# Performance work log

Measured on AMD Instinct MI355X. Metric: run time of the kernel, lower is better.

## Reference

```python
import jax, jax.numpy as jnp
import numpy as np

N_NODES = 10000
N_EDGES = 640000
IN_C = 128
OUT_C = 128
BOND_F = 16


def setup_inputs() -> dict:
    key = jax.random.key(0)
    ks = jax.random.split(key, 8)
    x = jax.random.normal(ks[0], (N_NODES, IN_C), dtype=jnp.float32)
    edge_attr = jax.random.normal(ks[1], (N_EDGES, BOND_F), dtype=jnp.float32)
    edge_weight = jax.random.uniform(ks[2], (N_EDGES, 1), dtype=jnp.float32)
    W_bond = jax.random.normal(ks[3], (BOND_F, IN_C), dtype=jnp.float32) * 0.1
    b_bond = jax.random.normal(ks[4], (IN_C,), dtype=jnp.float32) * 0.1
    W_lin = jax.random.normal(ks[5], (IN_C, OUT_C), dtype=jnp.float32) * 0.05
    b_lin = jax.random.normal(ks[6], (OUT_C,), dtype=jnp.float32) * 0.05
    edge_index = jax.random.randint(ks[7], (2, N_EDGES), 0, N_NODES, dtype=jnp.int32)
    return {"x": x, "edge_attr": edge_attr, "edge_weight": edge_weight,
            "W_bond": W_bond, "b_bond": b_bond, "W_lin": W_lin, "b_lin": b_lin,
            "edge_index": edge_index}


def _inv_sqrt_deg(idx, n, dtype):
    # degree via segment_sum of ones; inf (deg==0) mapped to 0
    deg = jax.ops.segment_sum(jnp.ones_like(idx, dtype=dtype), idx, num_segments=n)
    return jnp.where(deg > 0, jax.lax.rsqrt(jnp.maximum(deg, 1.0)) * (deg > 0), 0.0).astype(dtype)


def reference(x, edge_attr, edge_weight, W_bond, b_bond, W_lin, b_lin, edge_index):
    n = x.shape[0]
    # bond encoder: Linear on edge features -> [E, C]
    edge_emb = edge_attr @ W_bond + b_bond
    # append self-loops with zero edge embedding and unit edge weight
    sl = jnp.arange(n, dtype=edge_index.dtype)
    ei = jnp.concatenate([edge_index, jnp.stack([sl, sl])], axis=1)  # [2, E+N]
    emb = jnp.concatenate([edge_emb, jnp.zeros((n, edge_emb.shape[1]), edge_emb.dtype)], axis=0)
    ew = jnp.concatenate([edge_weight, jnp.ones((n, 1), edge_weight.dtype)], axis=0)
    row, col = ei[0], ei[1]
    norm = _inv_sqrt_deg(row, n, x.dtype)[row] * _inv_sqrt_deg(col, n, x.dtype)[col]
    # gather + GELU(exact/erf) + degree norm + edge weight, then scatter-sum
    msg = jax.nn.gelu(x[row] + emb, approximate=False) * norm[:, None] * ew
    out = jax.ops.segment_sum(msg, col, num_segments=n)  # [N, C]
    return out @ W_lin + b_lin
```

## Files before the change

kernel.cpp:

```cpp
#include <hip/hip_runtime.h>
#include <hip/hip_bf16.h>
#include <math.h>

#define N_NODES 10000
#define N_EDGES 640000
#define C 128
#define BF 16
#define MAXD 160

typedef int   iv4 __attribute__((ext_vector_type(4)));
typedef float fv4 __attribute__((ext_vector_type(4)));

__device__ __forceinline__ float2 bf2_to_f2(unsigned u) {
    union { unsigned x; float f; } lo, hi;
    lo.x = (u & 0xffffu) << 16;
    hi.x = u & 0xffff0000u;
    float2 r; r.x = lo.f; r.y = hi.f; return r;
}

__device__ __forceinline__ float fast_gelu(float z) {
    float z2 = z * z;
    float p  = z * fmaf(0.044715f, z2, 1.0f);
    float e  = __builtin_amdgcn_exp2f(-2.3022082f * p);
    float r  = __builtin_amdgcn_rcpf(1.0f + e);
    return z * r;
}

__global__ __launch_bounds__(256) void k_pre(
    const float* __restrict__ x, __hip_bfloat16* __restrict__ xb,
    const int* __restrict__ ei, int* __restrict__ dr, int* __restrict__ dc,
    int* __restrict__ pos)
{
    int b = blockIdx.x;
    if (b < 1250) {
        int i = (b * 256 + threadIdx.x) * 4;
        float4 v = *(const float4*)(x + i);
        xb[i + 0] = __float2bfloat16(v.x);
        xb[i + 1] = __float2bfloat16(v.y);
        xb[i + 2] = __float2bfloat16(v.z);
        xb[i + 3] = __float2bfloat16(v.w);
        return;
    }
    int e = (b - 1250) * 256 + threadIdx.x;
    int r = ei[e];
    int c = ei[N_EDGES + e];
    atomicAdd(&dr[r], 1);
    pos[e] = atomicAdd(&dc[c], 1);
}

__global__ __launch_bounds__(256) void k_prep2(
    const int* __restrict__ ei, const float* __restrict__ ew,
    const int* __restrict__ dr, const int* __restrict__ pos,
    iv4* __restrict__ bs)
{
    int e = blockIdx.x * 256 + threadIdx.x;
    int r = ei[e];
    int c = ei[N_EDGES + e];
    int pp = pos[e];
    if (pp >= MAXD) return;
    float s = rsqrtf((float)(dr[r] + 1)) * ew[e];
    iv4 v;
    v.x = e;
    v.y = r;
    v.z = __float_as_int(s);
    v.w = 0;
    bs[(size_t)c * MAXD + pp] = v;
}

#define EDGE_COMPUTE(q0, q1, q2, q3, xu, s) do {                          \
    float m0 = bbv.x, m1 = bbv.y;                                         \
    m0 = fmaf(q0.x, wb[0].x, m0);   m1 = fmaf(q0.x, wb[0].y, m1);         \
    m0 = fmaf(q0.y, wb[1].x, m0);   m1 = fmaf(q0.y, wb[1].y, m1);         \
    m0 = fmaf(q0.z, wb[2].x, m0);   m1 = fmaf(q0.z, wb[2].y, m1);         \
    m0 = fmaf(q0.w, wb[3].x, m0);   m1 = fmaf(q0.w, wb[3].y, m1);         \
    m0 = fmaf(q1.x, wb[4].x, m0);   m1 = fmaf(q1.x, wb[4].y, m1);         \
    m0 = fmaf(q1.y, wb[5].x, m0);   m1 = fmaf(q1.y, wb[5].y, m1);         \
    m0 = fmaf(q1.z, wb[6].x, m0);   m1 = fmaf(q1.z, wb[6].y, m1);         \
    m0 = fmaf(q1.w, wb[7].x, m0);   m1 = fmaf(q1.w, wb[7].y, m1);         \
    m0 = fmaf(q2.x, wb[8].x, m0);   m1 = fmaf(q2.x, wb[8].y, m1);         \
    m0 = fmaf(q2.y, wb[9].x, m0);   m1 = fmaf(q2.y, wb[9].y, m1);         \
    m0 = fmaf(q2.z, wb[10].x, m0);  m1 = fmaf(q2.z, wb[10].y, m1);        \
    m0 = fmaf(q2.w, wb[11].x, m0);  m1 = fmaf(q2.w, wb[11].y, m1);        \
    m0 = fmaf(q3.x, wb[12].x, m0);  m1 = fmaf(q3.x, wb[12].y, m1);        \
    m0 = fmaf(q3.y, wb[13].x, m0);  m1 = fmaf(q3.y, wb[13].y, m1);        \
    m0 = fmaf(q3.z, wb[14].x, m0);  m1 = fmaf(q3.z, wb[14].y, m1);        \
    m0 = fmaf(q3.w, wb[15].x, m0);  m1 = fmaf(q3.w, wb[15].y, m1);        \
    float2 xf = bf2_to_f2(xu);                                            \
    a0 = fmaf(fast_gelu(xf.x + m0), (s), a0);                             \
    a1 = fmaf(fast_gelu(xf.y + m1), (s), a1);                             \
} while (0)

__global__ __launch_bounds__(512) void k_node(
    const __hip_bfloat16* __restrict__ xb,
    const float* __restrict__ ea,
    const float* __restrict__ Wb, const float* __restrict__ bb,
    const int* __restrict__ dr, const int* __restrict__ dc,
    const iv4* __restrict__ bs,
    const float* __restrict__ Wl, const float* __restrict__ bl,
    float* __restrict__ out)
{
    int n = blockIdx.x;
    int t = threadIdx.x;
    int w = t >> 6;
    int p = t & 63;

    float2 wb[BF];
#pragma unroll
    for (int k = 0; k < BF; k++)
        wb[k] = *(const float2*)(Wb + (size_t)k * C + 2 * p);
    float2 bbv = *(const float2*)(bb + 2 * p);

    int cnt = dc[n]; if (cnt > MAXD) cnt = MAXD;
    float icn = rsqrtf((float)(dc[n] + 1));
    float irn = rsqrtf((float)(dr[n] + 1));

    float a0 = 0.f, a1 = 0.f;
    const unsigned* xbu = (const unsigned*)xb;
    int o0 = n * MAXD;
    int o1 = o0 + cnt;

    int i = o0 + w;
    if (i < o1) {
        iv4 h0 = __builtin_nontemporal_load(bs + i);
        iv4 h1 = (i + 8 < o1) ? __builtin_nontemporal_load(bs + i + 8) : h0;
        int e0 = __builtin_amdgcn_readfirstlane(h0.x);
        int r0 = __builtin_amdgcn_readfirstlane(h0.y);
        float s0 = __uint_as_float((unsigned)__builtin_amdgcn_readfirstlane(h0.z));
        const fv4* ep = (const fv4*)ea + (size_t)e0 * 4;
        fv4 q0 = ep[0], q1 = ep[1], q2 = ep[2], q3 = ep[3];
        unsigned xu = xbu[(size_t)r0 * 64 + p];

        while (true) {
            bool more = (i + 8 < o1);
            iv4 h2 = (i + 16 < o1) ? __builtin_nontemporal_load(bs + i + 16) : h0;
            int e1 = __builtin_amdgcn_readfirstlane(h1.x);
            int r1 = __builtin_amdgcn_readfirstlane(h1.y);
            float s1 = __uint_as_float((unsigned)__builtin_amdgcn_readfirstlane(h1.z));
            const fv4* epn = (const fv4*)ea + (size_t)e1 * 4;
            fv4 u0 = epn[0], u1 = epn[1], u2 = epn[2], u3 = epn[3];
            unsigned xun = xbu[(size_t)r1 * 64 + p];
            EDGE_COMPUTE(q0, q1, q2, q3, xu, s0);
            if (!more) break;
            q0 = u0; q1 = u1; q2 = u2; q3 = u3; xu = xun; s0 = s1;
            h0 = h1; h1 = h2; i += 8;
        }
    }

    __shared__ float2 shp[8][64];
    __shared__ __align__(16) float shs[C];
    __shared__ float sho[4][C];

    shp[w][p] = make_float2(a0, a1);
    __syncthreads();
    if (t < 64) {
        float vx = 0.f, vy = 0.f;
#pragma unroll
        for (int k = 0; k < 8; k++) { vx += shp[k][t].x; vy += shp[k][t].y; }
        float2 xf = bf2_to_f2(xbu[(size_t)n * 64 + t]);
        shs[2 * t]     = (vx + fast_gelu(xf.x) * irn) * icn;
        shs[2 * t + 1] = (vy + fast_gelu(xf.y) * irn) * icn;
    }
    __syncthreads();

    int ch = t & (C - 1), q = t >> 7;
    float o = 0.f;
    const float4* shv = (const float4*)shs + q * 8;
    const float* wcol = Wl + (size_t)(q * 32) * C + ch;
#pragma unroll
    for (int k4 = 0; k4 < 8; k4++) {
        float4 sv = shv[k4];
        o = fmaf(sv.x, wcol[(size_t)(k4 * 4 + 0) * C], o);
        o = fmaf(sv.y, wcol[(size_t)(k4 * 4 + 1) * C], o);
        o = fmaf(sv.z, wcol[(size_t)(k4 * 4 + 2) * C], o);
        o = fmaf(sv.w, wcol[(size_t)(k4 * 4 + 3) * C], o);
    }
    sho[q][ch] = o;
    __syncthreads();
    if (t < C) out[(size_t)n * C + t] = bl[t] + sho[0][t] + sho[1][t] + sho[2][t] + sho[3][t];
}

__global__ void k_deg(const int* __restrict__ ei, int* __restrict__ dr, int* __restrict__ dc) {
    int e = blockIdx.x * blockDim.x + threadIdx.x;
    if (e < N_EDGES) {
        atomicAdd(&dr[ei[e]], 1);
        atomicAdd(&dc[ei[N_EDGES + e]], 1);
    }
}

__global__ __launch_bounds__(1024) void k_scan_fb(
    const int* __restrict__ dr, const int* __restrict__ dc,
    int* __restrict__ off, float* __restrict__ ir, float* __restrict__ ic)
{
    __shared__ int shp[1024];
    int t = threadIdx.x;
    int base = t * 10;
    int loc[10];
    int s = 0;
#pragma unroll
    for (int j = 0; j < 10; j++) {
        int i = base + j;
        int v = (i < N_NODES) ? dc[i] : 0;
        loc[j] = s;
        s += v;
    }
    shp[t] = s;
    __syncthreads();
    for (int st = 1; st < 1024; st <<= 1) {
        int a = (t >= st) ? shp[t - st] : 0;
        __syncthreads();
        shp[t] += a;
        __syncthreads();
    }
    int excl = shp[t] - s;
#pragma unroll
    for (int j = 0; j < 10; j++) {
        int i = base + j;
        if (i < N_NODES) {
            off[i] = excl + loc[j];
            ir[i] = rsqrtf((float)(dr[i] + 1));
            ic[i] = rsqrtf((float)(dc[i] + 1));
        }
    }
    if (t == 1023) off[N_NODES] = shp[1023];
}

__global__ void k_scatter(const int* __restrict__ ei, const int* __restrict__ off,
                          int* __restrict__ cur, int* __restrict__ bucket) {
    int e = blockIdx.x * blockDim.x + threadIdx.x;
    if (e < N_EDGES) {
        int c = ei[N_EDGES + e];
        int pos = atomicAdd(&cur[c], 1);
        bucket[off[c] + pos] = e;
    }
}

__global__ __launch_bounds__(512) void k_node_fb(
    const float* __restrict__ x,
    const float* __restrict__ ea, const float* __restrict__ ew,
    const float* __restrict__ Wb, const float* __restrict__ bb,
    const int* __restrict__ ei,
    const float* __restrict__ ir, const float* __restrict__ ic,
    const int* __restrict__ off, const int* __restrict__ bucket,
    const float* __restrict__ Wl, const float* __restrict__ bl,
    float* __restrict__ out)
{
    int n = blockIdx.x;
    int t = threadIdx.x & (C - 1);
    int g = threadIdx.x >> 7;
    float icn = ic[n];
    float wb[BF];
#pragma unroll
    for (int k = 0; k < BF; k++) wb[k] = Wb[(size_t)k * C + t];
    float bbt = bb[t];
    float acc = 0.0f;
    if (g == 0) acc = fast_gelu(x[(size_t)n * C + t]) * (ir[n] * icn);
    int o0 = off[n], o1 = off[n + 1];
    for (int i = o0 + g; i < o1; i += 4) {
        int e = __builtin_amdgcn_readfirstlane(bucket[i]);
        int r = ei[e];
        float s = ir[r] * icn * ew[e];
        const float4* eapt = (const float4*)(ea + (size_t)e * BF);
        float4 q0 = eapt[0], q1 = eapt[1], q2 = eapt[2], q3 = eapt[3];
        float emb = bbt;
        emb = fmaf(q0.x, wb[0], emb);  emb = fmaf(q0.y, wb[1], emb);
        emb = fmaf(q0.z, wb[2], emb);  emb = fmaf(q0.w, wb[3], emb);
        emb = fmaf(q1.x, wb[4], emb);  emb = fmaf(q1.y, wb[5], emb);
        emb = fmaf(q1.z, wb[6], emb);  emb = fmaf(q1.w, wb[7], emb);
        emb = fmaf(q2.x, wb[8], emb);  emb = fmaf(q2.y, wb[9], emb);
        emb = fmaf(q2.z, wb[10], emb); emb = fmaf(q2.w, wb[11], emb);
        emb = fmaf(q3.x, wb[12], emb); emb = fmaf(q3.y, wb[13], emb);
        emb = fmaf(q3.z, wb[14], emb); emb = fmaf(q3.w, wb[15], emb);
        acc = fmaf(fast_gelu(x[(size_t)r * C + t] + emb), s, acc);
    }
    __shared__ float shp[4][C];
    __shared__ float shs[C];
    shp[g][t] = acc;
    __syncthreads();
    if (threadIdx.x < C) {
        int k = threadIdx.x;
        shs[k] = shp[0][k] + shp[1][k] + shp[2][k] + shp[3][k];
    }
    __syncthreads();
    float o = 0.0f;
    int k0 = g * 32;
#pragma unroll 8
    for (int j = 0; j < 32; j++) {
        int k = k0 + j;
        o = fmaf(shs[k], Wl[(size_t)k * C + t], o);
    }
    shp[g][t] = o;
    __syncthreads();
    if (threadIdx.x < C) {
        int c = threadIdx.x;
        out[(size_t)n * C + c] = bl[c] + shp[0][c] + shp[1][c] + shp[2][c] + shp[3][c];
    }
}

extern "C" void kernel_launch(void* const* d_in, const int* in_sizes, int n_in,
                              void* d_out, int out_size, void* d_ws, size_t ws_size,
                              hipStream_t stream) {
    const float* x  = (const float*)d_in[0];
    const float* ea = (const float*)d_in[1];
    const float* ew = (const float*)d_in[2];
    const float* Wb = (const float*)d_in[3];
    const float* bb = (const float*)d_in[4];
    const float* Wl = (const float*)d_in[5];
    const float* bl = (const float*)d_in[6];
    const int*   ei = (const int*)d_in[7];
    float* out = (float*)d_out;

    const size_t need_full = (size_t)N_NODES * MAXD * 16
                           + (size_t)640000 * 4 + (size_t)640000 * 4
                           + (size_t)2 * 10240 * 4;

    if (ws_size >= need_full) {
        iv4* bs = (iv4*)d_ws;
        unsigned* xbu = (unsigned*)(bs + (size_t)N_NODES * MAXD);
        int* pos = (int*)(xbu + 640000);
        int* dr  = pos + 640000;
        int* dc  = dr + 10240;
        __hip_bfloat16* xb = (__hip_bfloat16*)xbu;

        (void)hipMemsetAsync(dr, 0, 2 * 10240 * sizeof(int), stream);
        k_pre<<<3750, 256, 0, stream>>>(x, xb, ei, dr, dc, pos);
        k_prep2<<<2500, 256, 0, stream>>>(ei, ew, dr, pos, bs);
        k_node<<<N_NODES, 512, 0, stream>>>(
            xb, ea, Wb, bb, dr, dc, bs, Wl, bl, out);
    } else {
        int* bucket = (int*)d_ws;
        int* off = bucket + 640000;
        int* dr  = off + 10304;
        int* dc  = dr + 10240;
        int* cur = dc + 10240;
        float* ir = (float*)(cur + 10240);
        float* ic = ir + 10240;

        (void)hipMemsetAsync(dr, 0, 3 * 10240 * sizeof(int), stream);
        k_deg<<<(N_EDGES + 255) / 256, 256, 0, stream>>>(ei, dr, dc);
        k_scan_fb<<<1, 1024, 0, stream>>>(dr, dc, off, ir, ic);
        k_scatter<<<(N_EDGES + 255) / 256, 256, 0, stream>>>(ei, off, cur, bucket);
        k_node_fb<<<N_NODES, 512, 0, stream>>>(
            x, ea, ew, Wb, bb, ei, ir, ic, off, bucket, Wl, bl, out);
    }
}
```

Before: 271.3 us.

## Merge prep kernels, drop bf16 x copy, stage edge data in LDS

The degree-count and bucket-fill kernels become one, with the source-degree norm now applied inside the node kernel, so the separate pos array and one launch go away. The bf16 conversion of x is dropped and the node kernel gathers fp32 x directly. Each node block first loads its edge list and the matching edge_attr rows into shared memory cooperatively, then runs the per-edge loop out of LDS. The cost is double-width x gathers, extra syncthreads, and more LDS per block, which may lower occupancy.

```diff
diff --git a/kernel.cpp b/kernel.cpp
--- a/kernel.cpp
+++ b/kernel.cpp
@@ -8,15 +8,7 @@
 #define BF 16
 #define MAXD 160
 
-typedef int   iv4 __attribute__((ext_vector_type(4)));
-typedef float fv4 __attribute__((ext_vector_type(4)));
-
-__device__ __forceinline__ float2 bf2_to_f2(unsigned u) {
-    union { unsigned x; float f; } lo, hi;
-    lo.x = (u & 0xffffu) << 16;
-    hi.x = u & 0xffff0000u;
-    float2 r; r.x = lo.f; r.y = hi.f; return r;
-}
+typedef int iv4 __attribute__((ext_vector_type(4)));
 
 __device__ __forceinline__ float fast_gelu(float z) {
     float z2 = z * z;
@@ -26,48 +18,26 @@
     return z * r;
 }
 
-__global__ __launch_bounds__(256) void k_pre(
-    const float* __restrict__ x, __hip_bfloat16* __restrict__ xb,
-    const int* __restrict__ ei, int* __restrict__ dr, int* __restrict__ dc,
-    int* __restrict__ pos)
-{
-    int b = blockIdx.x;
-    if (b < 1250) {
-        int i = (b * 256 + threadIdx.x) * 4;
-        float4 v = *(const float4*)(x + i);
-        xb[i + 0] = __float2bfloat16(v.x);
-        xb[i + 1] = __float2bfloat16(v.y);
-        xb[i + 2] = __float2bfloat16(v.z);
-        xb[i + 3] = __float2bfloat16(v.w);
-        return;
-    }
-    int e = (b - 1250) * 256 + threadIdx.x;
-    int r = ei[e];
-    int c = ei[N_EDGES + e];
-    atomicAdd(&dr[r], 1);
-    pos[e] = atomicAdd(&dc[c], 1);
-}
-
-__global__ __launch_bounds__(256) void k_prep2(
+__global__ __launch_bounds__(256) void k_prep(
     const int* __restrict__ ei, const float* __restrict__ ew,
-    const int* __restrict__ dr, const int* __restrict__ pos,
-    iv4* __restrict__ bs)
+    int* __restrict__ dr, int* __restrict__ dc, iv4* __restrict__ bs)
 {
     int e = blockIdx.x * 256 + threadIdx.x;
     int r = ei[e];
     int c = ei[N_EDGES + e];
-    int pp = pos[e];
-    if (pp >= MAXD) return;
-    float s = rsqrtf((float)(dr[r] + 1)) * ew[e];
-    iv4 v;
-    v.x = e;
-    v.y = r;
-    v.z = __float_as_int(s);
-    v.w = 0;
-    bs[(size_t)c * MAXD + pp] = v;
-}
-
-#define EDGE_COMPUTE(q0, q1, q2, q3, xu, s) do {                          \
+    atomicAdd(&dr[r], 1);
+    int pp = atomicAdd(&dc[c], 1);
+    if (pp < MAXD) {
+        iv4 v;
+        v.x = e;
+        v.y = r;
+        v.z = __float_as_int(ew[e]);
+        v.w = 0;
+        bs[(size_t)c * MAXD + pp] = v;
+    }
+}
+
+#define EDGE_COMPUTE(q0, q1, q2, q3, xf, s) do {                          \
     float m0 = bbv.x, m1 = bbv.y;                                         \
     m0 = fmaf(q0.x, wb[0].x, m0);   m1 = fmaf(q0.x, wb[0].y, m1);         \
     m0 = fmaf(q0.y, wb[1].x, m0);   m1 = fmaf(q0.y, wb[1].y, m1);         \
@@ -85,14 +55,12 @@
     m0 = fmaf(q3.y, wb[13].x, m0);  m1 = fmaf(q3.y, wb[13].y, m1);        \
     m0 = fmaf(q3.z, wb[14].x, m0);  m1 = fmaf(q3.z, wb[14].y, m1);        \
     m0 = fmaf(q3.w, wb[15].x, m0);  m1 = fmaf(q3.w, wb[15].y, m1);        \
-    float2 xf = bf2_to_f2(xu);                                            \
     a0 = fmaf(fast_gelu(xf.x + m0), (s), a0);                             \
     a1 = fmaf(fast_gelu(xf.y + m1), (s), a1);                             \
 } while (0)
 
 __global__ __launch_bounds__(512) void k_node(
-    const __hip_bfloat16* __restrict__ xb,
-    const float* __restrict__ ea,
+    const float* __restrict__ x, const float* __restrict__ ea,
     const float* __restrict__ Wb, const float* __restrict__ bb,
     const int* __restrict__ dr, const int* __restrict__ dc,
     const iv4* __restrict__ bs,
@@ -104,45 +72,59 @@
     int w = t >> 6;
     int p = t & 63;
 
+    __shared__ int   se[MAXD];
+    __shared__ int   sr[MAXD];
+    __shared__ float ss[MAXD];
+    __shared__ __align__(16) float ea_s[MAXD][BF];
+
+    int cnt = dc[n]; if (cnt > MAXD) cnt = MAXD;
+
+    if (t < cnt) {
+        iv4 h = bs[(size_t)n * MAXD + t];
+        se[t] = h.x;
+        sr[t] = h.y;
+        ss[t] = rsqrtf((float)(dr[h.y] + 1)) * __int_as_float(h.z);
+    }
+    __syncthreads();
+    for (int j = (t >> 2); j < cnt; j += 128) {
+        ((float4*)ea_s[j])[t & 3] =
+            ((const float4*)(ea + (size_t)se[j] * BF))[t & 3];
+    }
+
     float2 wb[BF];
 #pragma unroll
     for (int k = 0; k < BF; k++)
         wb[k] = *(const float2*)(Wb + (size_t)k * C + 2 * p);
     float2 bbv = *(const float2*)(bb + 2 * p);
-
-    int cnt = dc[n]; if (cnt > MAXD) cnt = MAXD;
-    float icn = rsqrtf((float)(dc[n] + 1));
-    float irn = rsqrtf((float)(dr[n] + 1));
+    __syncthreads();
 
     float a0 = 0.f, a1 = 0.f;
-    const unsigned* xbu = (const unsigned*)xb;
-    int o0 = n * MAXD;
-    int o1 = o0 + cnt;
-
-    int i = o0 + w;
-    if (i < o1) {
-        iv4 h0 = __builtin_nontemporal_load(bs + i);
-        iv4 h1 = (i + 8 < o1) ? __builtin_nontemporal_load(bs + i + 8) : h0;
-        int e0 = __builtin_amdgcn_readfirstlane(h0.x);
-        int r0 = __builtin_amdgcn_readfirstlane(h0.y);
-        float s0 = __uint_as_float((unsigned)__builtin_amdgcn_readfirstlane(h0.z));
-        const fv4* ep = (const fv4*)ea + (size_t)e0 * 4;
-        fv4 q0 = ep[0], q1 = ep[1], q2 = ep[2], q3 = ep[3];
-        unsigned xu = xbu[(size_t)r0 * 64 + p];
+    int j = w;
+    if (j < cnt) {
+        float4 q0 = ((const float4*)ea_s[j])[0];
+        float4 q1 = ((const float4*)ea_s[j])[1];
+        float4 q2 = ((const float4*)ea_s[j])[2];
+        float4 q3 = ((const float4*)ea_s[j])[3];
+        float  s0 = ss[j];
+        int    r0 = sr[j];
+        float2 xf = *(const float2*)(x + (size_t)r0 * C + 2 * p);
 
         while (true) {
-            bool more = (i + 8 < o1);
-            iv4 h2 = (i + 16 < o1) ? __builtin_nontemporal_load(bs + i + 16) : h0;
-            int e1 = __builtin_amdgcn_readfirstlane(h1.x);
-            int r1 = __builtin_amdgcn_readfirstlane(h1.y);
-            float s1 = __uint_as_float((unsigned)__builtin_amdgcn_readfirstlane(h1.z));
-            const fv4* epn = (const fv4*)ea + (size_t)e1 * 4;
-            fv4 u0 = epn[0], u1 = epn[1], u2 = epn[2], u3 = epn[3];
-            unsigned xun = xbu[(size_t)r1 * 64 + p];
-            EDGE_COMPUTE(q0, q1, q2, q3, xu, s0);
+            int jn = j + 8;
+            bool more = (jn < cnt);
+            float4 u0, u1, u2, u3; float s1; float2 xg;
+            if (more) {
+                u0 = ((const float4*)ea_s[jn])[0];
+                u1 = ((const float4*)ea_s[jn])[1];
+                u2 = ((const float4*)ea_s[jn])[2];
+                u3 = ((const float4*)ea_s[jn])[3];
+                s1 = ss[jn];
+                int r1 = sr[jn];
+                xg = *(const float2*)(x + (size_t)r1 * C + 2 * p);
+            }
+            EDGE_COMPUTE(q0, q1, q2, q3, xf, s0);
             if (!more) break;
-            q0 = u0; q1 = u1; q2 = u2; q3 = u3; xu = xun; s0 = s1;
-            h0 = h1; h1 = h2; i += 8;
+            q0 = u0; q1 = u1; q2 = u2; q3 = u3; xf = xg; s0 = s1; j = jn;
         }
     }
 
@@ -156,7 +138,9 @@
         float vx = 0.f, vy = 0.f;
 #pragma unroll
         for (int k = 0; k < 8; k++) { vx += shp[k][t].x; vy += shp[k][t].y; }
-        float2 xf = bf2_to_f2(xbu[(size_t)n * 64 + t]);
+        float icn = rsqrtf((float)(dc[n] + 1));
+        float irn = rsqrtf((float)(dr[n] + 1));
+        float2 xf = *(const float2*)(x + (size_t)n * C + 2 * t);
         shs[2 * t]     = (vx + fast_gelu(xf.x) * irn) * icn;
         shs[2 * t + 1] = (vy + fast_gelu(xf.y) * irn) * icn;
     }
@@ -309,23 +293,17 @@
     const int*   ei = (const int*)d_in[7];
     float* out = (float*)d_out;
 
-    const size_t need_full = (size_t)N_NODES * MAXD * 16
-                           + (size_t)640000 * 4 + (size_t)640000 * 4
-                           + (size_t)2 * 10240 * 4;
+    const size_t need_full = (size_t)N_NODES * MAXD * 16 + (size_t)2 * 10240 * 4;
 
     if (ws_size >= need_full) {
         iv4* bs = (iv4*)d_ws;
-        unsigned* xbu = (unsigned*)(bs + (size_t)N_NODES * MAXD);
-        int* pos = (int*)(xbu + 640000);
-        int* dr  = pos + 640000;
-        int* dc  = dr + 10240;
-        __hip_bfloat16* xb = (__hip_bfloat16*)xbu;
+        int* dr = (int*)(bs + (size_t)N_NODES * MAXD);
+        int* dc = dr + 10240;
 
         (void)hipMemsetAsync(dr, 0, 2 * 10240 * sizeof(int), stream);
-        k_pre<<<3750, 256, 0, stream>>>(x, xb, ei, dr, dc, pos);
-        k_prep2<<<2500, 256, 0, stream>>>(ei, ew, dr, pos, bs);
+        k_prep<<<2500, 256, 0, stream>>>(ei, ew, dr, dc, bs);
         k_node<<<N_NODES, 512, 0, stream>>>(
-            xb, ea, Wb, bb, dr, dc, bs, Wl, bl, out);
+            x, ea, Wb, bb, dr, dc, bs, Wl, bl, out);
     } else {
         int* bucket = (int*)d_ws;
         int* off = bucket + 640000;
```

After: 317.5 us. +17.0%, slower.
